# Performance work log

Hardware: AMD Instinct MI355X
Metric: run time of the kernel (lower is better)

The kernel has to match this reference:

```python
import jax, jax.numpy as jnp
import numpy as np

B = 512
LIN = 96
LOUT = 96
NUM = 64      # numeric feature size (also decoder output size)
EMB = 32      # embedding dim
HID = 256     # GRU hidden size
VOCAB = 512
IN_SIZE = NUM + EMB


def setup_inputs() -> dict:
    key = jax.random.key(0)
    ks = jax.random.split(key, 9)
    s = 0.05
    return {
        "input_num": jax.random.normal(ks[0], (B, LIN + LOUT, NUM), dtype=jnp.float32),
        "input_cat": jax.random.randint(ks[1], (B, LIN + LOUT), 0, VOCAB),
        "emb_table": jax.random.normal(ks[2], (VOCAB, EMB), dtype=jnp.float32) * s,
        "W_ih": jax.random.normal(ks[3], (3 * HID, IN_SIZE), dtype=jnp.float32) * s,
        "W_hh": jax.random.normal(ks[4], (3 * HID, HID), dtype=jnp.float32) * s,
        "b_ih": jax.random.normal(ks[5], (3 * HID,), dtype=jnp.float32) * s,
        "b_hh": jax.random.normal(ks[6], (3 * HID,), dtype=jnp.float32) * s,
        "W_dec": jax.random.normal(ks[7], (NUM, HID), dtype=jnp.float32) * s,
        "b_dec": jax.random.normal(ks[8], (NUM,), dtype=jnp.float32) * s,
    }


def _gru_step(h, x, W_ih, W_hh, b_ih, b_hh):
    # PyTorch GRU cell math. h: [B,H], x: [B,in]
    H = h.shape[-1]
    gx = x @ W_ih.T + b_ih   # [B, 3H]
    gh = h @ W_hh.T + b_hh   # [B, 3H]
    r = jax.nn.sigmoid(gx[:, :H] + gh[:, :H])
    z = jax.nn.sigmoid(gx[:, H:2 * H] + gh[:, H:2 * H])
    n = jnp.tanh(gx[:, 2 * H:] + r * gh[:, 2 * H:])
    return (1.0 - z) * n + z * h


def reference(input_num, input_cat, emb_table, W_ih, W_hh, b_ih, b_hh, W_dec, b_dec):
    emb_seq = emb_table[input_cat]                      # [B, T, EMB]
    # ---- encoder over first LIN steps ----
    enc_in = jnp.concatenate([input_num[:, :LIN], emb_seq[:, :LIN]], axis=-1)
    h0 = jnp.zeros((input_num.shape[0], HID), dtype=input_num.dtype)

    def enc_body(h, x_t):
        return _gru_step(h, x_t, W_ih, W_hh, b_ih, b_hh), None

    h, _ = jax.lax.scan(enc_body, h0, jnp.swapaxes(enc_in, 0, 1))
    # single-layer GRU: output at last step == hidden state
    out0 = h @ W_dec.T + b_dec                          # [B, NUM]

    dec_emb = jnp.swapaxes(emb_seq[:, LIN:LIN + LOUT - 1], 0, 1)  # [LOUT-1, B, EMB]

    def dec_body(carry, e_t):
        h, out_prev = carry
        x = jnp.concatenate([out_prev, e_t], axis=-1)
        h_new = _gru_step(h, x, W_ih, W_hh, b_ih, b_hh)
        out = h_new @ W_dec.T + b_dec
        return (h_new, out), out

    _, outs = jax.lax.scan(dec_body, (h, out0), dec_emb)  # [LOUT-1, B, NUM]
    return jnp.concatenate([out0[:, None], jnp.swapaxes(outs, 0, 1)], axis=1)  # [B, LOUT, NUM]
```

## Files before the change

### kernel.cpp

```cpp
#include <hip/hip_runtime.h>


#define BATCH 512
#define TSEQ  192
#define LIN_  96
#define LOUT_ 96
#define NUM_  64
#define EMB_  32
#define HID_  256
#define INS_  96

#define NBLK  32
#define NT    512
#define XSTR  360

#define WS_WL   0u
#define WS_WS   98304u
#define WS_WD   245760u
#define WS_NEED 278528u

typedef __attribute__((ext_vector_type(8))) short short8_t;
typedef __attribute__((ext_vector_type(4))) float float4_t;
typedef unsigned short us;

__device__ __forceinline__ us f2bf(float x) {
    unsigned u = __builtin_bit_cast(unsigned, x);
    u = (u + 0x7FFFu + ((u >> 16) & 1u)) >> 16;
    return (us)u;
}
__device__ __forceinline__ float sigm(float x) {
    return __builtin_amdgcn_rcpf(1.0f + __builtin_amdgcn_exp2f(-1.44269504f * x));
}
__device__ __forceinline__ float tanhx(float x) {
    return 2.0f * __builtin_amdgcn_rcpf(1.0f + __builtin_amdgcn_exp2f(-2.88539008f * x)) - 1.0f;
}

__device__ __forceinline__ short8_t pack8(const float* v) {
    short8_t s;
    #pragma unroll
    for (int j = 0; j < 8; ++j) s[j] = (short)f2bf(v[j]);
    return s;
}

#define MFMA16(a, b, c) __builtin_amdgcn_mfma_f32_16x16x32_bf16((a), (b), (c), 0, 0, 0)

__global__ void prep_v10(const float* __restrict__ W_hh, const float* __restrict__ W_dec,
                         unsigned char* __restrict__ ws) {
    us* WLi = (us*)(ws + WS_WL);
    us* WSi = (us*)(ws + WS_WS);
    us* WDi = (us*)(ws + WS_WD);
    const int idx = blockIdx.x * 256 + threadIdx.x;
    if (idx >= 272 * 64) return;
    const int f = idx >> 6, l = idx & 63;
    const int r16 = l & 15, kq8 = (l >> 4) * 8;
    float tmp[8];
    if (f < 96) {
        const int g = f >> 5, rem = f & 31, tt = rem >> 1, cs = rem & 1;
        const int grow = g * 256 + tt * 16 + r16;
        const int k = (6 + cs) * 32 + kq8;
        #pragma unroll
        for (int j = 0; j < 8; ++j) tmp[j] = W_hh[(size_t)grow * HID_ + (k - INS_) + j];
        *(short8_t*)(WLi + (size_t)f * 512 + l * 8) = pack8(tmp);
    } else if (f < 240) {
        const int s = f - 96, g = s / 48, rem = s % 48, tt = rem / 3, cs = rem % 3;
        const int grow = g * 256 + tt * 16 + r16;
        const int k = (8 + cs) * 32 + kq8;
        #pragma unroll
        for (int j = 0; j < 8; ++j) tmp[j] = W_hh[(size_t)grow * HID_ + (k - INS_) + j];
        *(short8_t*)(WSi + (size_t)s * 512 + l * 8) = pack8(tmp);
    } else {
        const int f3 = f - 240, tt = f3 >> 3, c = f3 & 7;
        const int urow = tt * 16 + r16, k = c * 32 + kq8;
        #pragma unroll
        for (int j = 0; j < 8; ++j) tmp[j] = W_dec[(size_t)urow * HID_ + k + j];
        *(short8_t*)(WDi + (size_t)f3 * 512 + l * 8) = pack8(tmp);
    }
}

__global__ __launch_bounds__(NT, 2) void gru_v10(
    const float* __restrict__ input_num, const int* __restrict__ input_cat,
    const float* __restrict__ emb_table,
    const float* __restrict__ W_ih, const float* __restrict__ W_hh,
    const float* __restrict__ b_ih, const float* __restrict__ b_hh,
    const float* __restrict__ b_dec,
    const unsigned char* __restrict__ ws, float* __restrict__ out)
{
    __shared__ __align__(16) us XH[16 * XSTR];
    __shared__ __align__(16) us WLl[96 * 512];
    __shared__ __align__(16) us WDl[32 * 512];

    const us* WSf = (const us*)(ws + WS_WS);

    const int t = threadIdx.x, wave = t >> 6, lane = t & 63;
    const int arow = lane & 15, quad = lane >> 4, kq = quad * 8;
    const int bb = blockIdx.x * 16;
    const int tt0 = 2 * wave, tt1 = 2 * wave + 1;

    short8_t wfr[2][3][6];
    #pragma unroll
    for (int ti = 0; ti < 2; ++ti) {
        #pragma unroll
        for (int g3 = 0; g3 < 3; ++g3) {
            const int grow = g3 * HID_ + 32 * wave + 16 * ti + arow;
            #pragma unroll
            for (int kc = 0; kc < 6; ++kc) {
                float tmp[8];
                #pragma unroll
                for (int j2 = 0; j2 < 2; ++j2) {
                    const int k = kc * 32 + kq + j2 * 4;
                    float4 v = (k < INS_)
                        ? *(const float4*)&W_ih[(size_t)grow * INS_ + k]
                        : *(const float4*)&W_hh[(size_t)grow * HID_ + (k - INS_)];
                    tmp[j2 * 4 + 0] = v.x; tmp[j2 * 4 + 1] = v.y;
                    tmp[j2 * 4 + 2] = v.z; tmp[j2 * 4 + 3] = v.w;
                }
                wfr[ti][g3][kc] = pack8(tmp);
            }
        }
    }

    {
        const us* WLi = (const us*)(ws + WS_WL);
        const us* WDi = (const us*)(ws + WS_WD);
        for (int c = t; c < 96 * 64; c += NT)
            *(ulonglong2*)&WLl[c * 8] = *(const ulonglong2*)&WLi[c * 8];
        for (int c = t; c < 32 * 64; c += NT)
            *(ulonglong2*)&WDl[c * 8] = *(const ulonglong2*)&WDi[c * 8];
        for (int c = t; c < 16 * XSTR; c += NT) XH[c] = 0;
    }

    float bRr[2], bZr[2], bNXr[2], bNHr[2];
    #pragma unroll
    for (int ti = 0; ti < 2; ++ti) {
        const int u = 32 * wave + 16 * ti + arow;
        bRr[ti]  = b_ih[u] + b_hh[u];
        bZr[ti]  = b_ih[HID_ + u] + b_hh[HID_ + u];
        bNXr[ti] = b_ih[2 * HID_ + u];
        bNHr[ti] = b_hh[2 * HID_ + u];
    }
    const float bdr = (wave < 4) ? b_dec[wave * 16 + arow] : 0.0f;
    float hr[2][4] = {{0.f,0.f,0.f,0.f},{0.f,0.f,0.f,0.f}};
    __syncthreads();

    for (int sg = 1; sg <= 191; ++sg) {
        const int tstep = sg - 1;

        if (sg <= 96) {
            if (t < 256) {
                const int row = t >> 4, q = t & 15;
                float4 v = *(const float4*)&input_num[((size_t)(bb + row) * TSEQ + tstep) * NUM_ + q * 4];
                ushort4 s = { f2bf(v.x), f2bf(v.y), f2bf(v.z), f2bf(v.w) };
                *(ushort4*)&XH[row * XSTR + q * 4] = s;
            } else if (t < 384) {
                const int e = t - 256, row = e >> 3, q = e & 7;
                const int cat = input_cat[(bb + row) * TSEQ + tstep];
                float4 v = *(const float4*)&emb_table[cat * EMB_ + q * 4];
                ushort4 s = { f2bf(v.x), f2bf(v.y), f2bf(v.z), f2bf(v.w) };
                *(ushort4*)&XH[row * XSTR + NUM_ + q * 4] = s;
            }
        } else if (t < 128) {
            const int row = t >> 3, q = t & 7;
            const int cat = input_cat[(bb + row) * TSEQ + tstep];
            float4 v = *(const float4*)&emb_table[cat * EMB_ + q * 4];
            ushort4 s = { f2bf(v.x), f2bf(v.y), f2bf(v.z), f2bf(v.w) };
            *(ushort4*)&XH[row * XSTR + NUM_ + q * 4] = s;
        }
        __syncthreads();

        if (sg > 96) {
            if (wave < 4) {
                float4_t acc = {0.f, 0.f, 0.f, 0.f};
                #pragma unroll
                for (int c = 0; c < 8; ++c) {
                    short8_t b = *(const short8_t*)&WDl[(wave * 8 + c) * 512 + lane * 8];
                    short8_t a = *(const short8_t*)&XH[arow * XSTR + INS_ + c * 32 + kq];
                    acc = MFMA16(a, b, acc);
                }
                const int cg = wave * 16 + arow, pos = sg - 97;
                #pragma unroll
                for (int i = 0; i < 4; ++i) {
                    const int row = quad * 4 + i;
                    const float val = acc[i] + bdr;
                    XH[row * XSTR + cg] = f2bf(val);
                    out[((size_t)(bb + row) * LOUT_ + pos) * NUM_ + cg] = val;
                }
            }
            __syncthreads();
        }

        float4_t aR[2]  = {{0.f,0.f,0.f,0.f},{0.f,0.f,0.f,0.f}};
        float4_t aZ[2]  = {{0.f,0.f,0.f,0.f},{0.f,0.f,0.f,0.f}};
        float4_t aNX[2] = {{0.f,0.f,0.f,0.f},{0.f,0.f,0.f,0.f}};
        float4_t aNH[2] = {{0.f,0.f,0.f,0.f},{0.f,0.f,0.f,0.f}};

        short8_t s8[6], s9[6];
        #pragma unroll
        for (int g = 0; g < 3; ++g) {
            s8[g * 2 + 0] = *(const short8_t*)&WSf[(size_t)(g * 48 + tt0 * 3 + 0) * 512 + lane * 8];
            s8[g * 2 + 1] = *(const short8_t*)&WSf[(size_t)(g * 48 + tt1 * 3 + 0) * 512 + lane * 8];
            s9[g * 2 + 0] = *(const short8_t*)&WSf[(size_t)(g * 48 + tt0 * 3 + 1) * 512 + lane * 8];
            s9[g * 2 + 1] = *(const short8_t*)&WSf[(size_t)(g * 48 + tt1 * 3 + 1) * 512 + lane * 8];
        }

        #pragma unroll
        for (int kc = 0; kc < 6; ++kc) {
            short8_t a = *(const short8_t*)&XH[arow * XSTR + kc * 32 + kq];
            #pragma unroll
            for (int ti = 0; ti < 2; ++ti) {
                aR[ti] = MFMA16(a, wfr[ti][0][kc], aR[ti]);
                aZ[ti] = MFMA16(a, wfr[ti][1][kc], aZ[ti]);
                if (kc < 3) aNX[ti] = MFMA16(a, wfr[ti][2][kc], aNX[ti]);
                else        aNH[ti] = MFMA16(a, wfr[ti][2][kc], aNH[ti]);
            }
        }
        #pragma unroll
        for (int cs = 0; cs < 2; ++cs) {
            short8_t a = *(const short8_t*)&XH[arow * XSTR + (6 + cs) * 32 + kq];
            #pragma unroll
            for (int ti = 0; ti < 2; ++ti) {
                const int tt = tt0 + ti;
                short8_t b0 = *(const short8_t*)&WLl[(0 * 32 + tt * 2 + cs) * 512 + lane * 8];
                short8_t b1 = *(const short8_t*)&WLl[(1 * 32 + tt * 2 + cs) * 512 + lane * 8];
                short8_t b2 = *(const short8_t*)&WLl[(2 * 32 + tt * 2 + cs) * 512 + lane * 8];
                aR[ti] = MFMA16(a, b0, aR[ti]);
                aZ[ti] = MFMA16(a, b1, aZ[ti]);
                aNH[ti] = MFMA16(a, b2, aNH[ti]);
            }
        }
        short8_t s10[6];
        #pragma unroll
        for (int g = 0; g < 3; ++g) {
            s10[g * 2 + 0] = *(const short8_t*)&WSf[(size_t)(g * 48 + tt0 * 3 + 2) * 512 + lane * 8];
            s10[g * 2 + 1] = *(const short8_t*)&WSf[(size_t)(g * 48 + tt1 * 3 + 2) * 512 + lane * 8];
        }
        {
            short8_t a = *(const short8_t*)&XH[arow * XSTR + 8 * 32 + kq];
            #pragma unroll
            for (int ti = 0; ti < 2; ++ti) {
                aR[ti] = MFMA16(a, s8[0 * 2 + ti], aR[ti]);
                aZ[ti] = MFMA16(a, s8[1 * 2 + ti], aZ[ti]);
                aNH[ti] = MFMA16(a, s8[2 * 2 + ti], aNH[ti]);
            }
            a = *(const short8_t*)&XH[arow * XSTR + 9 * 32 + kq];
            #pragma unroll
            for (int ti = 0; ti < 2; ++ti) {
                aR[ti] = MFMA16(a, s9[0 * 2 + ti], aR[ti]);
                aZ[ti] = MFMA16(a, s9[1 * 2 + ti], aZ[ti]);
                aNH[ti] = MFMA16(a, s9[2 * 2 + ti], aNH[ti]);
            }
            a = *(const short8_t*)&XH[arow * XSTR + 10 * 32 + kq];
            #pragma unroll
            for (int ti = 0; ti < 2; ++ti) {
                aR[ti] = MFMA16(a, s10[0 * 2 + ti], aR[ti]);
                aZ[ti] = MFMA16(a, s10[1 * 2 + ti], aZ[ti]);
                aNH[ti] = MFMA16(a, s10[2 * 2 + ti], aNH[ti]);
            }
        }

        #pragma unroll
        for (int ti = 0; ti < 2; ++ti) {
            #pragma unroll
            for (int i = 0; i < 4; ++i) {
                const float r = sigm(aR[ti][i] + bRr[ti]);
                const float z = sigm(aZ[ti][i] + bZr[ti]);
                const float n = tanhx(aNX[ti][i] + bNXr[ti] + r * (aNH[ti][i] + bNHr[ti]));
                hr[ti][i] = (1.0f - z) * n + z * hr[ti][i];
            }
        }

        __syncthreads();
        #pragma unroll
        for (int ti = 0; ti < 2; ++ti) {
            #pragma unroll
            for (int i = 0; i < 4; ++i)
                XH[(quad * 4 + i) * XSTR + INS_ + 32 * wave + 16 * ti + arow] = f2bf(hr[ti][i]);
        }
    }

    __syncthreads();
    if (wave < 4) {
        float4_t acc = {0.f, 0.f, 0.f, 0.f};
        #pragma unroll
        for (int c = 0; c < 8; ++c) {
            short8_t b = *(const short8_t*)&WDl[(wave * 8 + c) * 512 + lane * 8];
            short8_t a = *(const short8_t*)&XH[arow * XSTR + INS_ + c * 32 + kq];
            acc = MFMA16(a, b, acc);
        }
        const int cg = wave * 16 + arow;
        #pragma unroll
        for (int i = 0; i < 4; ++i) {
            const int row = quad * 4 + i;
            out[((size_t)(bb + row) * LOUT_ + 95) * NUM_ + cg] = acc[i] + bdr;
        }
    }
}

__global__ __launch_bounds__(512) void gru_fallback(
    const float* __restrict__ input_num, const int* __restrict__ input_cat,
    const float* __restrict__ emb_table,
    const float* __restrict__ W_ih, const float* __restrict__ W_hh,
    const float* __restrict__ b_ih, const float* __restrict__ b_hh,
    const float* __restrict__ W_dec, const float* __restrict__ b_dec,
    float* __restrict__ out)
{
    __shared__ __align__(16) float xh[4][352];
    __shared__ float wdec[NUM_ * 257];
    const int t = threadIdx.x, bbase = blockIdx.x * 4;
    const int u = t & 255, rb = (t >> 8) * 2;
    for (int i = t; i < NUM_ * HID_; i += 512) wdec[(i >> 8) * 257 + (i & 255)] = W_dec[i];
    for (int i = t; i < 4 * HID_; i += 512) xh[i >> 8][INS_ + (i & 255)] = 0.0f;
    const float bR = b_ih[u] + b_hh[u], bZ = b_ih[256 + u] + b_hh[256 + u];
    const float bNX = b_ih[512 + u], bNH = b_hh[512 + u], bD = b_dec[t & 63];
    __syncthreads();
    auto sg_ = [](float x) { return 1.0f / (1.0f + __expf(-x)); };
    auto th_ = [](float x) { return 2.0f / (1.0f + __expf(-2.0f * x)) - 1.0f; };
    auto step = [&]() {
        float aR0 = bR, aR1 = bR, aZ0 = bZ, aZ1 = bZ, aNX0 = bNX, aNX1 = bNX, aNH0 = bNH, aNH1 = bNH;
        const float* x0 = xh[rb]; const float* x1 = xh[rb + 1];
        for (int kb = 0; kb < 88; ++kb) {
            float4 w0, w1, w2; int k4 = kb * 4;
            if (k4 < INS_) {
                w0 = *(const float4*)&W_ih[(size_t)u * INS_ + k4];
                w1 = *(const float4*)&W_ih[(size_t)(256 + u) * INS_ + k4];
                w2 = *(const float4*)&W_ih[(size_t)(512 + u) * INS_ + k4];
            } else {
                int kh = k4 - INS_;
                w0 = *(const float4*)&W_hh[(size_t)u * HID_ + kh];
                w1 = *(const float4*)&W_hh[(size_t)(256 + u) * HID_ + kh];
                w2 = *(const float4*)&W_hh[(size_t)(512 + u) * HID_ + kh];
            }
            float4 a = *(const float4*)&x0[k4], c = *(const float4*)&x1[k4];
            aR0 += w0.x*a.x+w0.y*a.y+w0.z*a.z+w0.w*a.w; aR1 += w0.x*c.x+w0.y*c.y+w0.z*c.z+w0.w*c.w;
            aZ0 += w1.x*a.x+w1.y*a.y+w1.z*a.z+w1.w*a.w; aZ1 += w1.x*c.x+w1.y*c.y+w1.z*c.z+w1.w*c.w;
            if (k4 < INS_) { aNX0 += w2.x*a.x+w2.y*a.y+w2.z*a.z+w2.w*a.w; aNX1 += w2.x*c.x+w2.y*c.y+w2.z*c.z+w2.w*c.w; }
            else           { aNH0 += w2.x*a.x+w2.y*a.y+w2.z*a.z+w2.w*a.w; aNH1 += w2.x*c.x+w2.y*c.y+w2.z*c.z+w2.w*c.w; }
        }
        float h0 = x0[INS_ + u], h1 = x1[INS_ + u];
        __syncthreads();
        { float r = sg_(aR0), z = sg_(aZ0), n = th_(aNX0 + r * aNH0);
          xh[rb][INS_ + u] = (1 - z) * n + z * h0; }
        { float r = sg_(aR1), z = sg_(aZ1), n = th_(aNX1 + r * aNH1);
          xh[rb + 1][INS_ + u] = (1 - z) * n + z * h1; }
        __syncthreads();
    };
    auto project = [&](int pos) {
        if (t < 256) {
            int r = t >> 6, m = t & 63;
            const float* wr = &wdec[m * 257]; const float* hr2 = &xh[r][INS_];
            float acc = bD;
            for (int k = 0; k < HID_; ++k) acc = fmaf(wr[k], hr2[k], acc);
            out[((size_t)(bbase + r) * LOUT_ + pos) * NUM_ + m] = acc;
            xh[r][m] = acc;
        }
    };
    for (int s = 0; s < LIN_; ++s) {
        if (t < 256) { int r = t >> 6, k = t & 63;
            xh[r][k] = input_num[((size_t)(bbase + r) * TSEQ + s) * NUM_ + k]; }
        if (t < 128) { int r = t >> 5, e = t & 31;
            xh[r][NUM_ + e] = emb_table[input_cat[(bbase + r) * TSEQ + s] * EMB_ + e]; }
        __syncthreads();
        step();
    }
    project(0);
    for (int s = 0; s < LOUT_ - 1; ++s) {
        if (t < 128) { int r = t >> 5, e = t & 31;
            xh[r][NUM_ + e] = emb_table[input_cat[(bbase + r) * TSEQ + LIN_ + s] * EMB_ + e]; }
        __syncthreads();
        step();
        project(s + 1);
    }
}

extern "C" void kernel_launch(void* const* d_in, const int* in_sizes, int n_in,
                              void* d_out, int out_size, void* d_ws, size_t ws_size,
                              hipStream_t stream) {
    const float* input_num = (const float*)d_in[0];
    const int*   input_cat = (const int*)d_in[1];
    const float* emb_table = (const float*)d_in[2];
    const float* W_ih      = (const float*)d_in[3];
    const float* W_hh      = (const float*)d_in[4];
    const float* b_ih      = (const float*)d_in[5];
    const float* b_hh      = (const float*)d_in[6];
    const float* W_dec     = (const float*)d_in[7];
    const float* b_dec     = (const float*)d_in[8];
    float* out = (float*)d_out;

    if (ws_size >= WS_NEED) {
        unsigned char* ws = (unsigned char*)d_ws;
        prep_v10<<<68, 256, 0, stream>>>(W_hh, W_dec, ws);
        gru_v10<<<NBLK, NT, 0, stream>>>(input_num, input_cat, emb_table,
                                         W_ih, W_hh, b_ih, b_hh, b_dec, ws, out);
    } else {
        gru_fallback<<<BATCH / 4, 512, 0, stream>>>(input_num, input_cat, emb_table,
                                                    W_ih, W_hh, b_ih, b_hh, W_dec, b_dec, out);
    }
}
```

Before: 967.8 us.

## Prefetch next-step inputs into registers and use LDS-only barriers

Input features and embedding rows for the next timestep are now loaded from global memory into registers one step ahead, and the category index two steps ahead. Only the bf16 conversion and the LDS store stay on the critical path. The __syncthreads calls are replaced with a barrier that waits only on LDS counters, so global loads and output stores can stay in flight across barriers. This adds register pressure and relies on the global loads not being needed before the barrier.

```diff
diff --git a/kernel.cpp b/kernel.cpp
--- a/kernel.cpp
+++ b/kernel.cpp
@@ -35,6 +35,13 @@
     return 2.0f * __builtin_amdgcn_rcpf(1.0f + __builtin_amdgcn_exp2f(-2.88539008f * x)) - 1.0f;
 }
 
+__device__ __forceinline__ void bar_lds() {
+    __builtin_amdgcn_sched_barrier(0);
+    asm volatile("s_waitcnt lgkmcnt(0)" ::: "memory");
+    __builtin_amdgcn_s_barrier();
+    __builtin_amdgcn_sched_barrier(0);
+}
+
 __device__ __forceinline__ short8_t pack8(const float* v) {
     short8_t s;
     #pragma unroll
@@ -44,7 +51,7 @@
 
 #define MFMA16(a, b, c) __builtin_amdgcn_mfma_f32_16x16x32_bf16((a), (b), (c), 0, 0, 0)
 
-__global__ void prep_v10(const float* __restrict__ W_hh, const float* __restrict__ W_dec,
+__global__ void prep_v11(const float* __restrict__ W_hh, const float* __restrict__ W_dec,
                          unsigned char* __restrict__ ws) {
     us* WLi = (us*)(ws + WS_WL);
     us* WSi = (us*)(ws + WS_WS);
@@ -77,7 +84,7 @@
     }
 }
 
-__global__ __launch_bounds__(NT, 2) void gru_v10(
+__global__ __launch_bounds__(NT, 2) void gru_v11(
     const float* __restrict__ input_num, const int* __restrict__ input_cat,
     const float* __restrict__ emb_table,
     const float* __restrict__ W_ih, const float* __restrict__ W_hh,
@@ -140,32 +147,41 @@
     }
     const float bdr = (wave < 4) ? b_dec[wave * 16 + arow] : 0.0f;
     float hr[2][4] = {{0.f,0.f,0.f,0.f},{0.f,0.f,0.f,0.f}};
+
+    const int srow = t >> 4, sq = t & 15;
+    const int erow = (t - 256) >> 3, eq = (t - 256) & 7;
+    const bool isN = (t < 256), isE = (t >= 256 && t < 384);
+    float4 pnum = {0.f,0.f,0.f,0.f}, pemb = {0.f,0.f,0.f,0.f};
+    int pcat = 0;
+    if (isN) {
+        pnum = *(const float4*)&input_num[((size_t)(bb + srow) * TSEQ + 0) * NUM_ + sq * 4];
+    } else if (isE) {
+        const int c0 = input_cat[(bb + erow) * TSEQ + 0];
+        pemb = *(const float4*)&emb_table[(size_t)c0 * EMB_ + eq * 4];
+        pcat = input_cat[(bb + erow) * TSEQ + 1];
+    }
     __syncthreads();
 
     for (int sg = 1; sg <= 191; ++sg) {
-        const int tstep = sg - 1;
-
         if (sg <= 96) {
-            if (t < 256) {
-                const int row = t >> 4, q = t & 15;
-                float4 v = *(const float4*)&input_num[((size_t)(bb + row) * TSEQ + tstep) * NUM_ + q * 4];
-                ushort4 s = { f2bf(v.x), f2bf(v.y), f2bf(v.z), f2bf(v.w) };
-                *(ushort4*)&XH[row * XSTR + q * 4] = s;
-            } else if (t < 384) {
-                const int e = t - 256, row = e >> 3, q = e & 7;
-                const int cat = input_cat[(bb + row) * TSEQ + tstep];
-                float4 v = *(const float4*)&emb_table[cat * EMB_ + q * 4];
-                ushort4 s = { f2bf(v.x), f2bf(v.y), f2bf(v.z), f2bf(v.w) };
-                *(ushort4*)&XH[row * XSTR + NUM_ + q * 4] = s;
-            }
-        } else if (t < 128) {
-            const int row = t >> 3, q = t & 7;
-            const int cat = input_cat[(bb + row) * TSEQ + tstep];
-            float4 v = *(const float4*)&emb_table[cat * EMB_ + q * 4];
-            ushort4 s = { f2bf(v.x), f2bf(v.y), f2bf(v.z), f2bf(v.w) };
-            *(ushort4*)&XH[row * XSTR + NUM_ + q * 4] = s;
-        }
-        __syncthreads();
+            if (isN) {
+                ushort4 s = { f2bf(pnum.x), f2bf(pnum.y), f2bf(pnum.z), f2bf(pnum.w) };
+                *(ushort4*)&XH[srow * XSTR + sq * 4] = s;
+            } else if (isE) {
+                ushort4 s = { f2bf(pemb.x), f2bf(pemb.y), f2bf(pemb.z), f2bf(pemb.w) };
+                *(ushort4*)&XH[erow * XSTR + NUM_ + eq * 4] = s;
+            }
+        } else if (isE) {
+            ushort4 s = { f2bf(pemb.x), f2bf(pemb.y), f2bf(pemb.z), f2bf(pemb.w) };
+            *(ushort4*)&XH[erow * XSTR + NUM_ + eq * 4] = s;
+        }
+        if (isN && sg <= 95)
+            pnum = *(const float4*)&input_num[((size_t)(bb + srow) * TSEQ + sg) * NUM_ + sq * 4];
+        if (isE && sg <= 190) {
+            pemb = *(const float4*)&emb_table[(size_t)pcat * EMB_ + eq * 4];
+            if (sg <= 189) pcat = input_cat[(bb + erow) * TSEQ + sg + 1];
+        }
+        bar_lds();
 
         if (sg > 96) {
             if (wave < 4) {
@@ -185,7 +201,7 @@
                     out[((size_t)(bb + row) * LOUT_ + pos) * NUM_ + cg] = val;
                 }
             }
-            __syncthreads();
+            bar_lds();
         }
 
         float4_t aR[2]  = {{0.f,0.f,0.f,0.f},{0.f,0.f,0.f,0.f}};
@@ -268,7 +284,7 @@
             }
         }
 
-        __syncthreads();
+        bar_lds();
         #pragma unroll
         for (int ti = 0; ti < 2; ++ti) {
             #pragma unroll
@@ -277,7 +293,7 @@
         }
     }
 
-    __syncthreads();
+    bar_lds();
     if (wave < 4) {
         float4_t acc = {0.f, 0.f, 0.f, 0.f};
         #pragma unroll
@@ -387,8 +403,8 @@
 
     if (ws_size >= WS_NEED) {
         unsigned char* ws = (unsigned char*)d_ws;
-        prep_v10<<<68, 256, 0, stream>>>(W_hh, W_dec, ws);
-        gru_v10<<<NBLK, NT, 0, stream>>>(input_num, input_cat, emb_table,
+        prep_v11<<<68, 256, 0, stream>>>(W_hh, W_dec, ws);
+        gru_v11<<<NBLK, NT, 0, stream>>>(input_num, input_cat, emb_table,
                                          W_ih, W_hh, b_ih, b_hh, b_dec, ws, out);
     } else {
         gru_fallback<<<BATCH / 4, 512, 0, stream>>>(input_num, input_cat, emb_table,
```

Measured after the change: 1.019 ms. 1.05x slower.

## Enlarge LDS weight cache and overlap decoder output with hidden-state MFMAs

Applied to the files above, without the earlier changes.

Grows the LDS weight buffer to hold three W_hh K-chunks, so fewer per-step weight fragments are read from global memory. In the decode phase the W_dec fragments are loaded into part of that buffer at the encoder/decoder boundary, and the z/n gates fall back to global reads. The MFMAs over hidden-state chunks are reordered to run before the barrier that waits for the decoder output feedback, so the extra sync overlaps with useful work. The prep kernel shrinks to packing only the remaining global chunks. The cost is a more complex, phase-dependent schedule and an in-loop LDS rewrite at step 96.

```diff
diff --git a/kernel.cpp b/kernel.cpp
--- a/kernel.cpp
+++ b/kernel.cpp
@@ -14,10 +14,7 @@
 #define NT    512
 #define XSTR  360
 
-#define WS_WL   0u
-#define WS_WS   98304u
-#define WS_WD   245760u
-#define WS_NEED 278528u
+#define WS_NEED 131072u
 
 typedef __attribute__((ext_vector_type(8))) short short8_t;
 typedef __attribute__((ext_vector_type(4))) float float4_t;
@@ -44,52 +41,35 @@
 
 #define MFMA16(a, b, c) __builtin_amdgcn_mfma_f32_16x16x32_bf16((a), (b), (c), 0, 0, 0)
 
-__global__ void prep_v10(const float* __restrict__ W_hh, const float* __restrict__ W_dec,
-                         unsigned char* __restrict__ ws) {
-    us* WLi = (us*)(ws + WS_WL);
-    us* WSi = (us*)(ws + WS_WS);
-    us* WDi = (us*)(ws + WS_WD);
+__global__ void prep_v13(const float* __restrict__ W_hh, unsigned char* __restrict__ ws) {
+    us* WSi = (us*)ws;
     const int idx = blockIdx.x * 256 + threadIdx.x;
-    if (idx >= 272 * 64) return;
+    if (idx >= 128 * 64) return;
     const int f = idx >> 6, l = idx & 63;
     const int r16 = l & 15, kq8 = (l >> 4) * 8;
+    int g3, ck, tt;
+    if (f < 16)      { ck = 8; g3 = 1; tt = f; }
+    else if (f < 32) { ck = 8; g3 = 2; tt = f - 16; }
+    else { const int j = f - 32; ck = 9 + j / 48; const int rem = j % 48; g3 = rem / 16; tt = rem % 16; }
+    const int grow = g3 * HID_ + tt * 16 + r16;
+    const int k = ck * 32 + kq8;
     float tmp[8];
-    if (f < 96) {
-        const int g = f >> 5, rem = f & 31, tt = rem >> 1, cs = rem & 1;
-        const int grow = g * 256 + tt * 16 + r16;
-        const int k = (6 + cs) * 32 + kq8;
-        #pragma unroll
-        for (int j = 0; j < 8; ++j) tmp[j] = W_hh[(size_t)grow * HID_ + (k - INS_) + j];
-        *(short8_t*)(WLi + (size_t)f * 512 + l * 8) = pack8(tmp);
-    } else if (f < 240) {
-        const int s = f - 96, g = s / 48, rem = s % 48, tt = rem / 3, cs = rem % 3;
-        const int grow = g * 256 + tt * 16 + r16;
-        const int k = (8 + cs) * 32 + kq8;
-        #pragma unroll
-        for (int j = 0; j < 8; ++j) tmp[j] = W_hh[(size_t)grow * HID_ + (k - INS_) + j];
-        *(short8_t*)(WSi + (size_t)s * 512 + l * 8) = pack8(tmp);
-    } else {
-        const int f3 = f - 240, tt = f3 >> 3, c = f3 & 7;
-        const int urow = tt * 16 + r16, k = c * 32 + kq8;
-        #pragma unroll
-        for (int j = 0; j < 8; ++j) tmp[j] = W_dec[(size_t)urow * HID_ + k + j];
-        *(short8_t*)(WDi + (size_t)f3 * 512 + l * 8) = pack8(tmp);
-    }
-}
-
-__global__ __launch_bounds__(NT, 2) void gru_v10(
+    #pragma unroll
+    for (int j = 0; j < 8; ++j) tmp[j] = W_hh[(size_t)grow * HID_ + (k - INS_) + j];
+    *(short8_t*)(WSi + (size_t)f * 512 + l * 8) = pack8(tmp);
+}
+
+__global__ __launch_bounds__(NT, 2) void gru_v13(
     const float* __restrict__ input_num, const int* __restrict__ input_cat,
     const float* __restrict__ emb_table,
     const float* __restrict__ W_ih, const float* __restrict__ W_hh,
     const float* __restrict__ b_ih, const float* __restrict__ b_hh,
-    const float* __restrict__ b_dec,
+    const float* __restrict__ W_dec, const float* __restrict__ b_dec,
     const unsigned char* __restrict__ ws, float* __restrict__ out)
 {
     __shared__ __align__(16) us XH[16 * XSTR];
-    __shared__ __align__(16) us WLl[96 * 512];
-    __shared__ __align__(16) us WDl[32 * 512];
-
-    const us* WSf = (const us*)(ws + WS_WS);
+    __shared__ __align__(16) us WL[144 * 512];
+    const us* WSf = (const us*)ws;
 
     const int t = threadIdx.x, wave = t >> 6, lane = t & 63;
     const int arow = lane & 15, quad = lane >> 4, kq = quad * 8;
@@ -119,15 +99,22 @@
         }
     }
 
-    {
-        const us* WLi = (const us*)(ws + WS_WL);
-        const us* WDi = (const us*)(ws + WS_WD);
-        for (int c = t; c < 96 * 64; c += NT)
-            *(ulonglong2*)&WLl[c * 8] = *(const ulonglong2*)&WLi[c * 8];
-        for (int c = t; c < 32 * 64; c += NT)
-            *(ulonglong2*)&WDl[c * 8] = *(const ulonglong2*)&WDi[c * 8];
-        for (int c = t; c < 16 * XSTR; c += NT) XH[c] = 0;
-    }
+    for (int i = t; i < 144 * 64; i += NT) {
+        const int f = i >> 6, l = i & 63;
+        const int r16 = l & 15, kq8 = (l >> 4) * 8;
+        int g3, ck;
+        if (f < 48)      { g3 = f >> 4;        ck = 6; }
+        else if (f < 96) { g3 = (f - 48) >> 4; ck = 7; }
+        else             { g3 = (f - 96) >> 4; ck = 8; }
+        const int tt = f & 15;
+        const int grow = g3 * HID_ + tt * 16 + r16;
+        const int k = ck * 32 + kq8;
+        float tmp[8];
+        #pragma unroll
+        for (int j = 0; j < 8; ++j) tmp[j] = W_hh[(size_t)grow * HID_ + (k - INS_) + j];
+        *(short8_t*)&WL[f * 512 + l * 8] = pack8(tmp);
+    }
+    for (int c = t; c < 16 * XSTR; c += NT) XH[c] = 0;
 
     float bRr[2], bZr[2], bNXr[2], bNHr[2];
     #pragma unroll
@@ -167,25 +154,22 @@
         }
         __syncthreads();
 
-        if (sg > 96) {
-            if (wave < 4) {
-                float4_t acc = {0.f, 0.f, 0.f, 0.f};
-                #pragma unroll
-                for (int c = 0; c < 8; ++c) {
-                    short8_t b = *(const short8_t*)&WDl[(wave * 8 + c) * 512 + lane * 8];
-                    short8_t a = *(const short8_t*)&XH[arow * XSTR + INS_ + c * 32 + kq];
-                    acc = MFMA16(a, b, acc);
-                }
-                const int cg = wave * 16 + arow, pos = sg - 97;
-                #pragma unroll
-                for (int i = 0; i < 4; ++i) {
-                    const int row = quad * 4 + i;
-                    const float val = acc[i] + bdr;
-                    XH[row * XSTR + cg] = f2bf(val);
-                    out[((size_t)(bb + row) * LOUT_ + pos) * NUM_ + cg] = val;
-                }
-            }
-            __syncthreads();
+        if (sg > 96 && wave < 4) {
+            float4_t acc = {0.f, 0.f, 0.f, 0.f};
+            #pragma unroll
+            for (int c = 0; c < 8; ++c) {
+                short8_t b = *(const short8_t*)&WL[(112 + wave * 8 + c) * 512 + lane * 8];
+                short8_t a = *(const short8_t*)&XH[arow * XSTR + INS_ + c * 32 + kq];
+                acc = MFMA16(a, b, acc);
+            }
+            const int cg = wave * 16 + arow, pos = sg - 97;
+            #pragma unroll
+            for (int i = 0; i < 4; ++i) {
+                const int row = quad * 4 + i;
+                const float val = acc[i] + bdr;
+                XH[row * XSTR + cg] = f2bf(val);
+                out[((size_t)(bb + row) * LOUT_ + pos) * NUM_ + cg] = val;
+            }
         }
 
         float4_t aR[2]  = {{0.f,0.f,0.f,0.f},{0.f,0.f,0.f,0.f}};
@@ -193,68 +177,110 @@
         float4_t aNX[2] = {{0.f,0.f,0.f,0.f},{0.f,0.f,0.f,0.f}};
         float4_t aNH[2] = {{0.f,0.f,0.f,0.f},{0.f,0.f,0.f,0.f}};
 
-        short8_t s8[6], s9[6];
+        short8_t s9[6];
         #pragma unroll
         for (int g = 0; g < 3; ++g) {
-            s8[g * 2 + 0] = *(const short8_t*)&WSf[(size_t)(g * 48 + tt0 * 3 + 0) * 512 + lane * 8];
-            s8[g * 2 + 1] = *(const short8_t*)&WSf[(size_t)(g * 48 + tt1 * 3 + 0) * 512 + lane * 8];
-            s9[g * 2 + 0] = *(const short8_t*)&WSf[(size_t)(g * 48 + tt0 * 3 + 1) * 512 + lane * 8];
-            s9[g * 2 + 1] = *(const short8_t*)&WSf[(size_t)(g * 48 + tt1 * 3 + 1) * 512 + lane * 8];
-        }
-
-        #pragma unroll
-        for (int kc = 0; kc < 6; ++kc) {
-            short8_t a = *(const short8_t*)&XH[arow * XSTR + kc * 32 + kq];
+            s9[g * 2 + 0] = *(const short8_t*)&WSf[(size_t)(32 + g * 16 + tt0) * 512 + lane * 8];
+            s9[g * 2 + 1] = *(const short8_t*)&WSf[(size_t)(32 + g * 16 + tt1) * 512 + lane * 8];
+        }
+        short8_t s8z[2], s8n[2];
+        if (sg > 96) {
+            s8z[0] = *(const short8_t*)&WSf[(size_t)(tt0) * 512 + lane * 8];
+            s8z[1] = *(const short8_t*)&WSf[(size_t)(tt1) * 512 + lane * 8];
+            s8n[0] = *(const short8_t*)&WSf[(size_t)(16 + tt0) * 512 + lane * 8];
+            s8n[1] = *(const short8_t*)&WSf[(size_t)(16 + tt1) * 512 + lane * 8];
+        }
+
+        short8_t a;
+        a = *(const short8_t*)&XH[arow * XSTR + 64 + kq];
+        #pragma unroll
+        for (int ti = 0; ti < 2; ++ti) {
+            aR[ti] = MFMA16(a, wfr[ti][0][2], aR[ti]);
+            aZ[ti] = MFMA16(a, wfr[ti][1][2], aZ[ti]);
+            aNX[ti] = MFMA16(a, wfr[ti][2][2], aNX[ti]);
+        }
+        #pragma unroll
+        for (int kc = 3; kc < 6; ++kc) {
+            a = *(const short8_t*)&XH[arow * XSTR + kc * 32 + kq];
             #pragma unroll
             for (int ti = 0; ti < 2; ++ti) {
                 aR[ti] = MFMA16(a, wfr[ti][0][kc], aR[ti]);
                 aZ[ti] = MFMA16(a, wfr[ti][1][kc], aZ[ti]);
-                if (kc < 3) aNX[ti] = MFMA16(a, wfr[ti][2][kc], aNX[ti]);
-                else        aNH[ti] = MFMA16(a, wfr[ti][2][kc], aNH[ti]);
+                aNH[ti] = MFMA16(a, wfr[ti][2][kc], aNH[ti]);
             }
         }
         #pragma unroll
         for (int cs = 0; cs < 2; ++cs) {
-            short8_t a = *(const short8_t*)&XH[arow * XSTR + (6 + cs) * 32 + kq];
+            a = *(const short8_t*)&XH[arow * XSTR + (6 + cs) * 32 + kq];
             #pragma unroll
             for (int ti = 0; ti < 2; ++ti) {
                 const int tt = tt0 + ti;
-                short8_t b0 = *(const short8_t*)&WLl[(0 * 32 + tt * 2 + cs) * 512 + lane * 8];
-                short8_t b1 = *(const short8_t*)&WLl[(1 * 32 + tt * 2 + cs) * 512 + lane * 8];
-                short8_t b2 = *(const short8_t*)&WLl[(2 * 32 + tt * 2 + cs) * 512 + lane * 8];
+                short8_t b0 = *(const short8_t*)&WL[(cs * 48 + 0 + tt) * 512 + lane * 8];
+                short8_t b1 = *(const short8_t*)&WL[(cs * 48 + 16 + tt) * 512 + lane * 8];
+                short8_t b2 = *(const short8_t*)&WL[(cs * 48 + 32 + tt) * 512 + lane * 8];
                 aR[ti] = MFMA16(a, b0, aR[ti]);
                 aZ[ti] = MFMA16(a, b1, aZ[ti]);
                 aNH[ti] = MFMA16(a, b2, aNH[ti]);
             }
         }
+        a = *(const short8_t*)&XH[arow * XSTR + 8 * 32 + kq];
+        if (sg <= 96) {
+            #pragma unroll
+            for (int ti = 0; ti < 2; ++ti) {
+                const int tt = tt0 + ti;
+                short8_t br = *(const short8_t*)&WL[(96 + tt) * 512 + lane * 8];
+                short8_t bz = *(const short8_t*)&WL[(112 + tt) * 512 + lane * 8];
+                short8_t bn = *(const short8_t*)&WL[(128 + tt) * 512 + lane * 8];
+                aR[ti] = MFMA16(a, br, aR[ti]);
+                aZ[ti] = MFMA16(a, bz, aZ[ti]);
+                aNH[ti] = MFMA16(a, bn, aNH[ti]);
+            }
+        } else {
+            #pragma unroll
+            for (int ti = 0; ti < 2; ++ti) {
+                const int tt = tt0 + ti;
+                short8_t br = *(const short8_t*)&WL[(96 + tt) * 512 + lane * 8];
+                aR[ti] = MFMA16(a, br, aR[ti]);
+                aZ[ti] = MFMA16(a, s8z[ti], aZ[ti]);
+                aNH[ti] = MFMA16(a, s8n[ti], aNH[ti]);
+            }
+        }
         short8_t s10[6];
         #pragma unroll
         for (int g = 0; g < 3; ++g) {
-            s10[g * 2 + 0] = *(const short8_t*)&WSf[(size_t)(g * 48 + tt0 * 3 + 2) * 512 + lane * 8];
-            s10[g * 2 + 1] = *(const short8_t*)&WSf[(size_t)(g * 48 + tt1 * 3 + 2) * 512 + lane * 8];
-        }
-        {
-            short8_t a = *(const short8_t*)&XH[arow * XSTR + 8 * 32 + kq];
-            #pragma unroll
-            for (int ti = 0; ti < 2; ++ti) {
-                aR[ti] = MFMA16(a, s8[0 * 2 + ti], aR[ti]);
-                aZ[ti] = MFMA16(a, s8[1 * 2 + ti], aZ[ti]);
-                aNH[ti] = MFMA16(a, s8[2 * 2 + ti], aNH[ti]);
-            }
-            a = *(const short8_t*)&XH[arow * XSTR + 9 * 32 + kq];
-            #pragma unroll
-            for (int ti = 0; ti < 2; ++ti) {
-                aR[ti] = MFMA16(a, s9[0 * 2 + ti], aR[ti]);
-                aZ[ti] = MFMA16(a, s9[1 * 2 + ti], aZ[ti]);
-                aNH[ti] = MFMA16(a, s9[2 * 2 + ti], aNH[ti]);
-            }
-            a = *(const short8_t*)&XH[arow * XSTR + 10 * 32 + kq];
-            #pragma unroll
-            for (int ti = 0; ti < 2; ++ti) {
-                aR[ti] = MFMA16(a, s10[0 * 2 + ti], aR[ti]);
-                aZ[ti] = MFMA16(a, s10[1 * 2 + ti], aZ[ti]);
-                aNH[ti] = MFMA16(a, s10[2 * 2 + ti], aNH[ti]);
-            }
+            s10[g * 2 + 0] = *(const short8_t*)&WSf[(size_t)(80 + g * 16 + tt0) * 512 + lane * 8];
+            s10[g * 2 + 1] = *(const short8_t*)&WSf[(size_t)(80 + g * 16 + tt1) * 512 + lane * 8];
+        }
+        a = *(const short8_t*)&XH[arow * XSTR + 9 * 32 + kq];
+        #pragma unroll
+        for (int ti = 0; ti < 2; ++ti) {
+            aR[ti] = MFMA16(a, s9[0 * 2 + ti], aR[ti]);
+            aZ[ti] = MFMA16(a, s9[1 * 2 + ti], aZ[ti]);
+            aNH[ti] = MFMA16(a, s9[2 * 2 + ti], aNH[ti]);
+        }
+        a = *(const short8_t*)&XH[arow * XSTR + 10 * 32 + kq];
+        #pragma unroll
+        for (int ti = 0; ti < 2; ++ti) {
+            aR[ti] = MFMA16(a, s10[0 * 2 + ti], aR[ti]);
+            aZ[ti] = MFMA16(a, s10[1 * 2 + ti], aZ[ti]);
+            aNH[ti] = MFMA16(a, s10[2 * 2 + ti], aNH[ti]);
+        }
+
+        if (sg > 96) __syncthreads();
+
+        a = *(const short8_t*)&XH[arow * XSTR + kq];
+        #pragma unroll
+        for (int ti = 0; ti < 2; ++ti) {
+            aR[ti] = MFMA16(a, wfr[ti][0][0], aR[ti]);
+            aZ[ti] = MFMA16(a, wfr[ti][1][0], aZ[ti]);
+            aNX[ti] = MFMA16(a, wfr[ti][2][0], aNX[ti]);
+        }
+        a = *(const short8_t*)&XH[arow * XSTR + 32 + kq];
+        #pragma unroll
+        for (int ti = 0; ti < 2; ++ti) {
+            aR[ti] = MFMA16(a, wfr[ti][0][1], aR[ti]);
+            aZ[ti] = MFMA16(a, wfr[ti][1][1], aZ[ti]);
+            aNX[ti] = MFMA16(a, wfr[ti][2][1], aNX[ti]);
         }
 
         #pragma unroll
@@ -275,6 +301,18 @@
             for (int i = 0; i < 4; ++i)
                 XH[(quad * 4 + i) * XSTR + INS_ + 32 * wave + 16 * ti + arow] = f2bf(hr[ti][i]);
         }
+
+        if (sg == 96) {
+            for (int i = t; i < 32 * 64; i += NT) {
+                const int f = i >> 6, l = i & 63;
+                const int w = f >> 3, c = f & 7;
+                const int urow = w * 16 + (l & 15), k = c * 32 + (l >> 4) * 8;
+                float tmp[8];
+                #pragma unroll
+                for (int j = 0; j < 8; ++j) tmp[j] = W_dec[(size_t)urow * HID_ + k + j];
+                *(short8_t*)&WL[(112 + f) * 512 + l * 8] = pack8(tmp);
+            }
+        }
     }
 
     __syncthreads();
@@ -282,7 +320,7 @@
         float4_t acc = {0.f, 0.f, 0.f, 0.f};
         #pragma unroll
         for (int c = 0; c < 8; ++c) {
-            short8_t b = *(const short8_t*)&WDl[(wave * 8 + c) * 512 + lane * 8];
+            short8_t b = *(const short8_t*)&WL[(112 + wave * 8 + c) * 512 + lane * 8];
             short8_t a = *(const short8_t*)&XH[arow * XSTR + INS_ + c * 32 + kq];
             acc = MFMA16(a, b, acc);
         }
@@ -387,9 +425,9 @@
 
     if (ws_size >= WS_NEED) {
         unsigned char* ws = (unsigned char*)d_ws;
-        prep_v10<<<68, 256, 0, stream>>>(W_hh, W_dec, ws);
-        gru_v10<<<NBLK, NT, 0, stream>>>(input_num, input_cat, emb_table,
-                                         W_ih, W_hh, b_ih, b_hh, b_dec, ws, out);
+        prep_v13<<<32, 256, 0, stream>>>(W_hh, ws);
+        gru_v13<<<NBLK, NT, 0, stream>>>(input_num, input_cat, emb_table,
+                                         W_ih, W_hh, b_ih, b_hh, W_dec, b_dec, ws, out);
     } else {
         gru_fallback<<<BATCH / 4, 512, 0, stream>>>(input_num, input_cat, emb_table,
                                                     W_ih, W_hh, b_ih, b_hh, W_dec, b_dec, out);
```

Result: slower. 1.177 ms (+21.6%).
